# Kernel optimization log

Hardware: AMD Instinct MI355X
Metric: run time of the kernel (lower is better)

Reference implementation:

```python
import jax, jax.numpy as jnp
import numpy as np
import math
from math import factorial

L = 3            # SH degree -> (L+1)^2 = 16 basis functions
H = 1024         # coefficient grid height
W = 1024         # coefficient grid width
B = 1048576      # number of rays (1024x1024 render)


def _norm_lm(l, m):
    return math.sqrt((2 * l + 1) / (4 * math.pi) * (factorial(l - m) / factorial(l + m)))


def real_spherical_harmonics(dirs, L):
    """dirs: [N,3] float32 -> [N,(L+1)^2] float32 real SH basis."""
    eps = 1e-14
    r = jnp.linalg.norm(dirs, axis=-1) + eps
    xd, yd, zd = dirs[:, 0], dirs[:, 1], dirs[:, 2]
    theta = jnp.arccos(jnp.clip(zd / r, -1.0, 1.0))
    phi = jnp.arctan2(yd, xd)
    ct = jnp.cos(theta)
    # Associated Legendre P_l^m(ct) via the standard recursion (loops over the
    # small fixed (l,m) set unroll at trace time; all ops vectorized over N).
    p = {(0, 0): jnp.ones_like(ct)}
    if L >= 1:
        p[(1, 0)] = ct
        s = jnp.sqrt(jnp.clip(1.0 - ct * ct, 1e-14, None))
        p[(1, 1)] = s
        for l in range(2, L + 1):
            p[(l, l)] = (2 * l - 1) * s * p[(l - 1, l - 1)]
            for m in range(l - 1, -1, -1):
                a = (2 * l - 1) * ct * p[(l - 1, m)]
                b = (l + m - 1) * p[(l - 2, m)] if (l - 2) >= m else 0.0
                p[(l, m)] = (a - b) / (l - m)
    cols = []
    sqrt2 = math.sqrt(2.0)
    for l in range(L + 1):
        for m in range(-l, l + 1):
            if m == 0:
                cols.append(_norm_lm(l, 0) * p[(l, 0)])
            elif m > 0:
                sign = (-1.0) ** m
                cols.append(sqrt2 * sign * _norm_lm(l, m) * p[(l, m)] * jnp.cos(m * phi))
            else:
                mp = -m
                sign = (-1.0) ** m
                cols.append(sqrt2 * sign * _norm_lm(l, mp) * p[(l, mp)] * jnp.sin(mp * phi))
    return jnp.stack(cols, axis=-1)  # [N, (L+1)^2]


def setup_inputs() -> dict:
    key = jax.random.key(0)
    k1, k2, k3, k4 = jax.random.split(key, 4)
    return {
        "y": jax.random.randint(k1, (B,), 0, H),
        "x": jax.random.randint(k2, (B,), 0, W),
        "ray_dir": jax.random.normal(k3, (B, 3), dtype=jnp.float32),
        "sh_data": 0.1 * jax.random.normal(k4, (H, W, (L + 1) ** 2, 3), dtype=jnp.float32),
    }


def reference(y, x, ray_dir, sh_data):
    coefs = sh_data[y, x]                       # [B, (L+1)^2, 3] gather
    B_mat = real_spherical_harmonics(ray_dir, L)  # [B, (L+1)^2]
    c = jnp.einsum('bi,bij->bj', B_mat, coefs)    # [B, 3]
    return jnp.clip(c, 0.0, 1.0)
```

## Files before the change

kernel.cpp:

```cpp
#include <hip/hip_runtime.h>


#define SH_C0   0.28209479177387814f
#define SH_C1   0.48860251190291992f
#define SH_C2a  1.09254843059207907f
#define SH_C2b  0.31539156525252005f
#define SH_C2c  0.54627421529603959f
#define SH_C3a  0.59004358992664352f
#define SH_C3b  2.89061144264055405f
#define SH_C3c  0.45704579946446572f
#define SH_C3d  0.37317633259011546f
#define SH_C3e  1.44530572132027702f

#define DO4(v, J0,C0, J1,C1, J2,C2, J3,C3)        \
    s##C0 = fmaf(b[J0], (v).x, s##C0);            \
    s##C1 = fmaf(b[J1], (v).y, s##C1);            \
    s##C2 = fmaf(b[J2], (v).z, s##C2);            \
    s##C3 = fmaf(b[J3], (v).w, s##C3);

__global__ __launch_bounds__(256) void sh_embed_coop(
    const int* __restrict__ ys, const int* __restrict__ xs,
    const float* __restrict__ dirs, const float* __restrict__ sh,
    float* __restrict__ out, int B)
{
    const int tid  = blockIdx.x * 256 + threadIdx.x;
    const int ray  = tid >> 2;
    const int q    = tid & 3;
    if (ray >= B) return;

    const int yy = ys[ray];
    const int xx = xs[ray];
    const float4* __restrict__ c4 =
        (const float4*)(sh + (size_t)(yy * 1024 + xx) * 48u);

    const float4 v0 = c4[q];
    const float4 v1 = c4[q + 4];
    const float4 v2 = c4[q + 8];

    const float dx = dirs[3 * ray + 0];
    const float dy = dirs[3 * ray + 1];
    const float dz = dirs[3 * ray + 2];
    const float inv = rsqrtf(fmaf(dx, dx, fmaf(dy, dy, dz * dz)));
    const float nx = dx * inv, ny = dy * inv, nz = dz * inv;

    const float x2 = nx * nx, y2 = ny * ny, z2 = nz * nz;
    const float xy = nx * ny, yz = ny * nz, xz = nx * nz;

    float b[16];
    b[0]  =  SH_C0;
    b[1]  = -SH_C1 * ny;
    b[2]  =  SH_C1 * nz;
    b[3]  = -SH_C1 * nx;
    b[4]  =  SH_C2a * xy;
    b[5]  = -SH_C2a * yz;
    b[6]  =  SH_C2b * (3.0f * z2 - 1.0f);
    b[7]  = -SH_C2a * xz;
    b[8]  =  SH_C2c * (x2 - y2);
    b[9]  = -SH_C3a * ny * (3.0f * x2 - y2);
    b[10] =  SH_C3b * xy * nz;
    b[11] = -SH_C3c * ny * (5.0f * z2 - 1.0f);
    b[12] =  SH_C3d * nz * (5.0f * z2 - 3.0f);
    b[13] = -SH_C3c * nx * (5.0f * z2 - 1.0f);
    b[14] =  SH_C3e * nz * (x2 - y2);
    b[15] = -SH_C3a * nx * (x2 - 3.0f * y2);

    float s0 = 0.0f, s1 = 0.0f, s2 = 0.0f;
    switch (q) {
    case 0:
        DO4(v0,  0,0,  0,1,  0,2,  1,0)
        DO4(v1,  5,1,  5,2,  6,0,  6,1)
        DO4(v2, 10,2, 11,0, 11,1, 11,2)
        break;
    case 1:
        DO4(v0,  1,1,  1,2,  2,0,  2,1)
        DO4(v1,  6,2,  7,0,  7,1,  7,2)
        DO4(v2, 12,0, 12,1, 12,2, 13,0)
        break;
    case 2:
        DO4(v0,  2,2,  3,0,  3,1,  3,2)
        DO4(v1,  8,0,  8,1,  8,2,  9,0)
        DO4(v2, 13,1, 13,2, 14,0, 14,1)
        break;
    default:
        DO4(v0,  4,0,  4,1,  4,2,  5,0)
        DO4(v1,  9,1,  9,2, 10,0, 10,1)
        DO4(v2, 14,2, 15,0, 15,1, 15,2)
        break;
    }

    s0 += __shfl_xor(s0, 1, 64);  s0 += __shfl_xor(s0, 2, 64);
    s1 += __shfl_xor(s1, 1, 64);  s1 += __shfl_xor(s1, 2, 64);
    s2 += __shfl_xor(s2, 1, 64);  s2 += __shfl_xor(s2, 2, 64);

    if (q < 3) {
        float val = (q == 0) ? s0 : (q == 1) ? s1 : s2;
        out[(size_t)3 * ray + q] = fminf(fmaxf(val, 0.0f), 1.0f);
    }
}

extern "C" void kernel_launch(void* const* d_in, const int* in_sizes, int n_in,
                              void* d_out, int out_size, void* d_ws, size_t ws_size,
                              hipStream_t stream) {
    const int*   ys   = (const int*)d_in[0];
    const int*   xs   = (const int*)d_in[1];
    const float* dirs = (const float*)d_in[2];
    const float* sh   = (const float*)d_in[3];
    float* out = (float*)d_out;
    int B = in_sizes[0];
    int blocks = (B + 63) / 64;
    sh_embed_coop<<<blocks, 256, 0, stream>>>(ys, xs, dirs, sh, out, B);
}
```

Before: 287.1 us.

## Process two rays per thread group with async global-to-LDS prefetch of second ray

Each group of 4 threads now handles two rays, one from each half of the batch. The second ray's coefficient gather is issued as asynchronous global_load_lds into shared memory while the first ray is computed, and a vmcnt wait precedes its use. The intent is more memory-level parallelism per thread to hide the latency of the random gather, at the cost of half the grid size, extra LDS usage and a leftover dead macro definition.

Result: no change. 289.3 us (+0.7%).

```diff
diff --git a/kernel.cpp b/kernel.cpp
--- a/kernel.cpp
+++ b/kernel.cpp
@@ -13,40 +13,22 @@
 #define SH_C3e  1.44530572132027702f
 
 #define DO4(v, J0,C0, J1,C1, J2,C2, J3,C3)        \
+    s0_ = fmaf(b[J0], (v).x, s0_), (void)0;       \
+    DO4_##C0                                       \
+
+#undef DO4
+#define DO4(v, J0,C0, J1,C1, J2,C2, J3,C3)        \
     s##C0 = fmaf(b[J0], (v).x, s##C0);            \
     s##C1 = fmaf(b[J1], (v).y, s##C1);            \
     s##C2 = fmaf(b[J2], (v).z, s##C2);            \
     s##C3 = fmaf(b[J3], (v).w, s##C3);
 
-__global__ __launch_bounds__(256) void sh_embed_coop(
-    const int* __restrict__ ys, const int* __restrict__ xs,
-    const float* __restrict__ dirs, const float* __restrict__ sh,
-    float* __restrict__ out, int B)
+__device__ __forceinline__ void sh_basis(float dx, float dy, float dz, float b[16])
 {
-    const int tid  = blockIdx.x * 256 + threadIdx.x;
-    const int ray  = tid >> 2;
-    const int q    = tid & 3;
-    if (ray >= B) return;
-
-    const int yy = ys[ray];
-    const int xx = xs[ray];
-    const float4* __restrict__ c4 =
-        (const float4*)(sh + (size_t)(yy * 1024 + xx) * 48u);
-
-    const float4 v0 = c4[q];
-    const float4 v1 = c4[q + 4];
-    const float4 v2 = c4[q + 8];
-
-    const float dx = dirs[3 * ray + 0];
-    const float dy = dirs[3 * ray + 1];
-    const float dz = dirs[3 * ray + 2];
     const float inv = rsqrtf(fmaf(dx, dx, fmaf(dy, dy, dz * dz)));
     const float nx = dx * inv, ny = dy * inv, nz = dz * inv;
-
     const float x2 = nx * nx, y2 = ny * ny, z2 = nz * nz;
     const float xy = nx * ny, yz = ny * nz, xz = nx * nz;
-
-    float b[16];
     b[0]  =  SH_C0;
     b[1]  = -SH_C1 * ny;
     b[2]  =  SH_C1 * nz;
@@ -63,7 +45,12 @@
     b[13] = -SH_C3c * nx * (5.0f * z2 - 1.0f);
     b[14] =  SH_C3e * nz * (x2 - y2);
     b[15] = -SH_C3a * nx * (x2 - 3.0f * y2);
+}
 
+__device__ __forceinline__ void sh_accum(int q, const float b[16],
+                                         float4 v0, float4 v1, float4 v2,
+                                         float& s0o, float& s1o, float& s2o)
+{
     float s0 = 0.0f, s1 = 0.0f, s2 = 0.0f;
     switch (q) {
     case 0:
@@ -87,6 +74,62 @@
         DO4(v2, 14,2, 15,0, 15,1, 15,2)
         break;
     }
+    s0o = s0; s1o = s1; s2o = s2;
+}
+
+__global__ __launch_bounds__(256, 8) void sh_embed_coop2(
+    const int* __restrict__ ys, const int* __restrict__ xs,
+    const float* __restrict__ dirs, const float* __restrict__ sh,
+    float* __restrict__ out, int B)
+{
+    __shared__ float lds[4][3][256];
+
+    const int tid  = threadIdx.x;
+    const int gid  = blockIdx.x * 256 + tid;
+    const int q    = tid & 3;
+    const int half = (B + 1) >> 1;
+    const int rayA = gid >> 2;
+    if (rayA >= half) return;
+    const int  rayB = rayA + half;
+    const bool hasB = (rayB < B);
+
+    const int yA = ys[rayA];
+    const int xA = xs[rayA];
+    int yB = 0, xB = 0;
+    if (hasB) { yB = ys[rayB]; xB = xs[rayB]; }
+
+    const float dA0 = dirs[3 * rayA + 0];
+    const float dA1 = dirs[3 * rayA + 1];
+    const float dA2 = dirs[3 * rayA + 2];
+    float dB0 = 0.f, dB1 = 0.f, dB2 = 0.f;
+    if (hasB) { dB0 = dirs[3 * rayB + 0]; dB1 = dirs[3 * rayB + 1]; dB2 = dirs[3 * rayB + 2]; }
+
+    const float4* __restrict__ c4A =
+        (const float4*)(sh + (size_t)(yA * 1024 + xA) * 48u);
+    const float4 vA0 = c4A[q];
+    const float4 vA1 = c4A[q + 4];
+    const float4 vA2 = c4A[q + 8];
+
+    const int wave = tid >> 6;
+    const int lane = tid & 63;
+    if (hasB) {
+        const float* gB = sh + (size_t)(yB * 1024 + xB) * 48u + 4 * q;
+        __builtin_amdgcn_global_load_lds(
+            (const __attribute__((address_space(1))) void*)(gB),
+            (__attribute__((address_space(3))) void*)&lds[wave][0][4 * lane], 16, 0, 0);
+        __builtin_amdgcn_global_load_lds(
+            (const __attribute__((address_space(1))) void*)(gB + 16),
+            (__attribute__((address_space(3))) void*)&lds[wave][1][4 * lane], 16, 0, 0);
+        __builtin_amdgcn_global_load_lds(
+            (const __attribute__((address_space(1))) void*)(gB + 32),
+            (__attribute__((address_space(3))) void*)&lds[wave][2][4 * lane], 16, 0, 0);
+    }
+
+    float b[16];
+    sh_basis(dA0, dA1, dA2, b);
+
+    float s0, s1, s2;
+    sh_accum(q, b, vA0, vA1, vA2, s0, s1, s2);
 
     s0 += __shfl_xor(s0, 1, 64);  s0 += __shfl_xor(s0, 2, 64);
     s1 += __shfl_xor(s1, 1, 64);  s1 += __shfl_xor(s1, 2, 64);
@@ -94,7 +137,28 @@
 
     if (q < 3) {
         float val = (q == 0) ? s0 : (q == 1) ? s1 : s2;
-        out[(size_t)3 * ray + q] = fminf(fmaxf(val, 0.0f), 1.0f);
+        out[(size_t)3 * rayA + q] = fminf(fmaxf(val, 0.0f), 1.0f);
+    }
+
+    if (hasB) {
+        asm volatile("s_waitcnt vmcnt(0)" ::: "memory");
+        __builtin_amdgcn_sched_barrier(0);
+
+        const float4 vB0 = *(const float4*)&lds[wave][0][4 * lane];
+        const float4 vB1 = *(const float4*)&lds[wave][1][4 * lane];
+        const float4 vB2 = *(const float4*)&lds[wave][2][4 * lane];
+
+        sh_basis(dB0, dB1, dB2, b);
+        sh_accum(q, b, vB0, vB1, vB2, s0, s1, s2);
+
+        s0 += __shfl_xor(s0, 1, 64);  s0 += __shfl_xor(s0, 2, 64);
+        s1 += __shfl_xor(s1, 1, 64);  s1 += __shfl_xor(s1, 2, 64);
+        s2 += __shfl_xor(s2, 1, 64);  s2 += __shfl_xor(s2, 2, 64);
+
+        if (q < 3) {
+            float val = (q == 0) ? s0 : (q == 1) ? s1 : s2;
+            out[(size_t)3 * rayB + q] = fminf(fmaxf(val, 0.0f), 1.0f);
+        }
     }
 }
 
@@ -107,6 +171,7 @@
     const float* sh   = (const float*)d_in[3];
     float* out = (float*)d_out;
     int B = in_sizes[0];
-    int blocks = (B + 63) / 64;
-    sh_embed_coop<<<blocks, 256, 0, stream>>>(ys, xs, dirs, sh, out, B);
+    int half   = (B + 1) >> 1;
+    int blocks = (half + 63) / 64;
+    sh_embed_coop2<<<blocks, 256, 0, stream>>>(ys, xs, dirs, sh, out, B);
 }
```
